# Performance work log

Measured on AMD Instinct MI355X. Metric: run time of the kernel, lower is better.

The kernel has to match this reference:

```python
import jax, jax.numpy as jnp
import numpy as np

B, S, D, H, NL, V, E, DFF = 4, 512, 768, 12, 2, 32000, 8, 3072
CF = 1.25
HD = D // H


def setup_inputs() -> dict:
    key = jax.random.key(0)
    ks = jax.random.split(key, 12)
    r = lambda i, shape: jax.random.normal(ks[i], shape, jnp.float32) * 0.02
    return {
        "src": jax.random.randint(ks[0], (B, S), 0, V),
        "src_pad_mask": jnp.zeros((B, S), bool),
        "emb": r(1, (V, D)),
        "qkv_w": r(2, (NL, 3 * D, D)), "qkv_b": jnp.zeros((NL, 3 * D), jnp.float32),
        "out_w": r(3, (NL, D, D)), "out_b": jnp.zeros((NL, D), jnp.float32),
        "wr": r(4, (NL, D, E)),
        "w1": r(5, (NL, E, D, DFF)), "b1": jnp.zeros((NL, E, DFF), jnp.float32),
        "w2": r(6, (NL, E, DFF, D)), "b2": jnp.zeros((NL, E, D), jnp.float32),
        "ln1_g": jnp.ones((NL, D), jnp.float32), "ln1_b": jnp.zeros((NL, D), jnp.float32),
        "ln2_g": jnp.ones((NL, D), jnp.float32), "ln2_b": jnp.zeros((NL, D), jnp.float32),
        "lnf_g": jnp.ones((D,), jnp.float32), "lnf_b": jnp.zeros((D,), jnp.float32),
    }


def layernorm(x, g, b, eps=1e-5):
    mu = jnp.mean(x, -1, keepdims=True)
    var = jnp.mean((x - mu) ** 2, -1, keepdims=True)
    return (x - mu) * jax.lax.rsqrt(var + eps) * g + b


def pos_encoding():
    pos = jnp.arange(S, dtype=jnp.float32)[:, None]
    i = jnp.arange(0, D, 2, dtype=jnp.float32)
    ang = pos * jnp.exp(-(i / D) * jnp.log(jnp.float32(10000.0)))  # [S, D/2]
    pe = jnp.zeros((S, D), jnp.float32)
    pe = pe.at[:, 0::2].set(jnp.sin(ang)).at[:, 1::2].set(jnp.cos(ang))
    return pe


def mha(x, wqkv, bqkv, wo, bo, pad):
    qkv = x @ wqkv.T + bqkv
    q, k, v = jnp.split(qkv, 3, axis=-1)
    q = q.reshape(B, S, H, HD); k = k.reshape(B, S, H, HD); v = v.reshape(B, S, H, HD)
    sc = jnp.einsum('bqhd,bkhd->bhqk', q, k) * (1.0 / float(HD) ** 0.5)
    sc = jnp.where(pad[:, None, None, :], jnp.float32(-1e9), sc)
    at = jax.nn.softmax(sc, -1)
    o = jnp.einsum('bhqk,bkhd->bqhd', at, v).reshape(B, S, D)
    return o @ wo.T + bo


def switch_ffn(x, token_mask, wr, w1, b1, w2, b2):
    # Switch Transformer top-1 routing with capacity drop.
    T = B * S
    cap = int(CF * T / E)
    xf = x.reshape(T, D)
    vm = token_mask.reshape(T).astype(x.dtype)
    logits = xf @ wr                                   # [T, E]
    probs = jax.nn.softmax(logits, -1)
    idx = jnp.argmax(probs, -1)
    gate = jnp.take_along_axis(probs, idx[:, None], -1)[:, 0]
    oh = jax.nn.one_hot(idx, E, dtype=x.dtype) * vm[:, None]      # [T, E]
    pos = jnp.cumsum(oh, axis=0) * oh                  # 1-indexed position in expert
    keep = ((pos > 0) & (pos <= cap)).astype(x.dtype)
    disp = keep[:, :, None] * jax.nn.one_hot((pos - 1).astype(jnp.int32), cap, dtype=x.dtype)  # [T,E,C]
    comb = disp * gate[:, None, None]
    ein = jnp.einsum('tec,td->ecd', disp, xf)          # [E, C, D]
    hid = jax.nn.relu(jnp.einsum('ecd,edf->ecf', ein, w1) + b1[:, None, :])
    eo = jnp.einsum('ecf,efd->ecd', hid, w2) + b2[:, None, :]
    y = jnp.einsum('tec,ecd->td', comb, eo).reshape(B, S, D)
    denom = jnp.maximum(vm.sum(), 1.0)
    me = (probs * vm[:, None]).sum(0) / denom
    ce = oh.sum(0) / denom
    lb = jnp.float32(E) * jnp.sum(me * ce)
    z = jnp.sum((jax.nn.logsumexp(logits, -1) ** 2) * vm) / denom
    return y, lb, z


def forward(src, src_pad_mask, emb, qkv_w, qkv_b, out_w, out_b, wr, w1, b1, w2, b2,
            ln1_g, ln1_b, ln2_g, ln2_b, lnf_g, lnf_b):
    x = emb[src] * jnp.float32(float(D) ** 0.5) + pos_encoding()[None]
    token_mask = ~src_pad_mask
    lbs, zs = [], []
    for l in range(NL):
        xn = layernorm(x, ln1_g[l], ln1_b[l])
        x = x + mha(xn, qkv_w[l], qkv_b[l], out_w[l], out_b[l], src_pad_mask)
        xn = layernorm(x, ln2_g[l], ln2_b[l])
        y, lb, z = switch_ffn(xn, token_mask, wr[l], w1[l], b1[l], w2[l], b2[l])
        x = x + y
        lbs.append(lb); zs.append(z)
    x = layernorm(x, lnf_g, lnf_b)
    return x, jnp.stack(lbs).mean(), jnp.stack(zs).mean()


def reference(src, src_pad_mask, emb, qkv_w, qkv_b, out_w, out_b, wr, w1, b1, w2, b2,
              ln1_g, ln1_b, ln2_g, ln2_b, lnf_g, lnf_b):
    return forward(src, src_pad_mask, emb, qkv_w, qkv_b, out_w, out_b, wr, w1, b1, w2, b2,
                   ln1_g, ln1_b, ln2_g, ln2_b, lnf_g, lnf_b)
```

## Files before the change

kernel.cpp:

```cpp
#include <hip/hip_runtime.h>

#define BB 4
#define SS 512
#define DD 768
#define HH 12
#define NLAYER 2
#define EE 8
#define DFF 3072
#define TT 2048
#define CAP 320
#define HD 64

typedef unsigned short u16;
typedef long long ll;
typedef _Float16 f16x8 __attribute__((ext_vector_type(8)));
typedef float f32x4 __attribute__((ext_vector_type(4)));

union F16U { _Float16 h; u16 u; };

__device__ __forceinline__ void split2h(float v, u16& h0, u16& h1) {
    F16U c0; c0.h = (_Float16)v;
    float r = (v - (float)c0.h) * 4096.0f;
    F16U c1; c1.h = (_Float16)r;
    h0 = c0.u; h1 = c1.u;
}
__device__ __forceinline__ float rec2h(u16 a, u16 b) {
    F16U c0, c1; c0.u = a; c1.u = b;
    return (float)c0.h + (float)c1.h * (1.0f / 4096.0f);
}

#define MFMA16(a, b, c) __builtin_amdgcn_mfma_f32_16x16x32_f16(a, b, c, 0, 0, 0)

struct GemmP {
    const u16* A = nullptr; ll sAp = 0;
    const void* B = nullptr; ll sBp = 0;
    const float* bias = nullptr; ll biasStride = 0;
    void* C = nullptr; ll sCp = 0;
    int M = 0, N = 0, K = 0, lda = 0, ldb = 0, ldc = 0;
    int modA = 1; ll sA1 = 0, sA2 = 0;
    int modB = 1; ll sB1 = 0, sB2 = 0;
    int modC = 1; ll sC1 = 0, sC2 = 0;
    float alpha = 1.f;
    int flags = 0;
    int KS = 1; ll partStride = 0;
    int Jc = 1;
};

#define BK 64
#define PADK 72

template<bool BTRANS, int NS>
__global__ __launch_bounds__(256) void gemm_kernel(GemmP p) {
    __shared__ u16 Al[NS][128][PADK];
    __shared__ u16 Bl[NS][128][PADK];
    const int tid = threadIdx.x;

    int bx, by, bz;
    {
        int gx = gridDim.x, gy = gridDim.y;
        int NBt = gx * gy * gridDim.z;
        int L = blockIdx.x + gx * (blockIdx.y + gy * blockIdx.z);
        int q = NBt >> 3, r = NBt & 7;
        int xcd = L & 7, wi = L >> 3;
        int c = (xcd < r) ? xcd * (q + 1) + wi : r * (q + 1) + (xcd - r) * q + wi;
        int Jc = p.Jc;
        int gxJ = gx * Jc;
        int sj = c / gxJ;
        int t = c - sj * gxJ;
        bx = t / Jc;
        int j = sj * Jc + (t - (t / Jc) * Jc);
        by = j % gy; bz = j / gy;
    }
    const int n0 = bx * 128, m0 = by * 128;
    const int slice = bz % p.KS;
    const int z = bz / p.KS;
    const int kslice = p.K / p.KS;
    const int k0 = slice * kslice;
    const int nkt = kslice >> 6;

    const u16* Ap = p.A + (ll)(z % p.modA) * p.sA1 + (ll)(z / p.modA) * p.sA2 + k0;
    const ll zB = (ll)(z % p.modB) * p.sB1 + (ll)(z / p.modB) * p.sB2;
    const ll zC = (ll)(z % p.modC) * p.sC1 + (ll)(z / p.modC) * p.sC2;
    const u16* Bpu = BTRANS ? ((const u16*)p.B + zB + k0) : nullptr;
    const float* Bpf = BTRANS ? nullptr : ((const float*)p.B + zB);

    const int lane = tid & 63, wid = tid >> 6;
    const int wm = (wid >> 1) * 64, wn = (wid & 1) * 64;
    const int ar = lane & 15, kg = (lane >> 4) * 8;

    f32x4 acc0[4][4] = {};
    f32x4 acc1[4][4] = {};

    uint4 ra[4 * NS];
    uint4 rb[4 * NS];
    float rbf[32];

    auto loadA = [&](int kt) {
        #pragma unroll
        for (int s = 0; s < NS; ++s)
            #pragma unroll
            for (int h = 0; h < 4; ++h) {
                int c = tid + h * 256, row = c >> 3, q = c & 7;
                int gm = m0 + row;
                uint4 v = {0u, 0u, 0u, 0u};
                if (gm < p.M) v = *(const uint4*)(Ap + (ll)s * p.sAp + (size_t)gm * p.lda + kt * BK + q * 8);
                ra[s * 4 + h] = v;
            }
    };
    auto storeA = [&]() {
        #pragma unroll
        for (int s = 0; s < NS; ++s)
            #pragma unroll
            for (int h = 0; h < 4; ++h) {
                int c = tid + h * 256, row = c >> 3, q = c & 7;
                *(uint4*)&Al[s][row][q * 8] = ra[s * 4 + h];
            }
    };
    auto loadB = [&](int kt) {
        if (BTRANS) {
            #pragma unroll
            for (int s = 0; s < NS; ++s)
                #pragma unroll
                for (int h = 0; h < 4; ++h) {
                    int c = tid + h * 256, row = c >> 3, q = c & 7;
                    int gn = n0 + row;
                    uint4 v = {0u, 0u, 0u, 0u};
                    if (gn < p.N) v = *(const uint4*)(Bpu + (ll)s * p.sBp + (size_t)gn * p.ldb + kt * BK + q * 8);
                    rb[s * 4 + h] = v;
                }
        } else {
            int gn = n0 + (tid & 127);
            int kb = (tid >> 7) * 32;
            #pragma unroll
            for (int i = 0; i < 32; ++i) {
                float v = 0.f;
                if (gn < p.N) v = Bpf[(size_t)(k0 + kt * BK + kb + i) * p.ldb + gn];
                rbf[i] = v;
            }
        }
    };
    auto storeB = [&]() {
        if (BTRANS) {
            #pragma unroll
            for (int s = 0; s < NS; ++s)
                #pragma unroll
                for (int h = 0; h < 4; ++h) {
                    int c = tid + h * 256, row = c >> 3, q = c & 7;
                    *(uint4*)&Bl[s][row][q * 8] = rb[s * 4 + h];
                }
        } else {
            int col = tid & 127;
            int kb = (tid >> 7) * 32;
            #pragma unroll
            for (int i = 0; i < 8; ++i) {
                u16 t0[4], t1[4];
                #pragma unroll
                for (int e = 0; e < 4; ++e) split2h(rbf[i * 4 + e], t0[e], t1[e]);
                *(uint2*)&Bl[0][col][kb + i * 4] = *(uint2*)t0;
                if (NS == 2) *(uint2*)&Bl[1][col][kb + i * 4] = *(uint2*)t1;
            }
        }
    };

    loadA(0); loadB(0);
    for (int kt = 0; kt < nkt; ++kt) {
        storeA(); storeB();
        __syncthreads();
        if (kt + 1 < nkt) { loadA(kt + 1); loadB(kt + 1); }
        #pragma unroll
        for (int kt2 = 0; kt2 < 2; ++kt2) {
            f16x8 b0r[4], b1r[4];
            #pragma unroll
            for (int j = 0; j < 4; ++j) {
                b0r[j] = *(const f16x8*)&Bl[0][wn + j * 16 + ar][kt2 * 32 + kg];
                if (NS == 2) b1r[j] = *(const f16x8*)&Bl[1][wn + j * 16 + ar][kt2 * 32 + kg];
            }
            #pragma unroll
            for (int i = 0; i < 4; ++i) {
                f16x8 a0 = *(const f16x8*)&Al[0][wm + i * 16 + ar][kt2 * 32 + kg];
                f16x8 a1;
                if (NS == 2) a1 = *(const f16x8*)&Al[1][wm + i * 16 + ar][kt2 * 32 + kg];
                #pragma unroll
                for (int j = 0; j < 4; ++j) {
                    acc0[i][j] = MFMA16(a0, b0r[j], acc0[i][j]);
                    if (NS == 2) {
                        acc1[i][j] = MFMA16(a0, b1r[j], acc1[i][j]);
                        acc1[i][j] = MFMA16(a1, b0r[j], acc1[i][j]);
                    }
                }
            }
        }
        __syncthreads();
    }

    const bool doPart = (p.flags & 16);
    float* Cpart = doPart ? ((float*)p.C + (ll)slice * p.partStride + zC) : nullptr;
    const float* biasp = (p.flags & 1) ? (p.bias + (ll)z * p.biasStride) : nullptr;
    u16* C0 = (!doPart && (p.flags & 8)) ? ((u16*)p.C + zC) : nullptr;
    u16* C1 = C0 ? (C0 + p.sCp) : nullptr;
    float* Cf = (!doPart && !(p.flags & 8)) ? ((float*)p.C + zC) : nullptr;
    #pragma unroll
    for (int i = 0; i < 4; ++i) {
        #pragma unroll
        for (int j = 0; j < 4; ++j) {
            int gc = n0 + wn + j * 16 + (lane & 15);
            if (gc >= p.N) continue;
            int gr0 = m0 + wm + i * 16 + (lane >> 4) * 4;
            #pragma unroll
            for (int r = 0; r < 4; ++r) {
                int gr = gr0 + r;
                if (gr >= p.M) continue;
                float v = acc0[i][j][r];
                if (NS == 2) v += acc1[i][j][r] * (1.0f / 4096.0f);
                v *= p.alpha;
                size_t off = (size_t)gr * p.ldc + gc;
                if (doPart) { Cpart[off] = v; continue; }
                if (p.flags & 1) v = __fadd_rn(v, biasp[gc]);
                if (p.flags & 2) v = fmaxf(v, 0.f);
                if (p.flags & 8) { u16 h0, h1; split2h(v, h0, h1); C0[off] = h0; C1[off] = h1; }
                else Cf[off] = v;
            }
        }
    }
}

struct WtP {
    const float* in; u16* out;
    int R, C;
    ll sIn, sOutZ, planeStride;
    int np;
};
__global__ void wtrans_kernel(WtP p) {
    __shared__ float t[32][33];
    int z = blockIdx.z;
    const float* in = p.in + (ll)z * p.sIn;
    u16* out = p.out + (ll)z * p.sOutZ;
    int c0 = blockIdx.x * 32, r0 = blockIdx.y * 32;
    int tx = threadIdx.x, ty = threadIdx.y;
    #pragma unroll
    for (int i = 0; i < 32; i += 8)
        t[ty + i][tx] = in[(size_t)(r0 + ty + i) * p.C + c0 + tx];
    __syncthreads();
    #pragma unroll
    for (int i = 0; i < 32; i += 8) {
        float v = t[tx][ty + i];
        size_t o = (size_t)(c0 + ty + i) * p.R + r0 + tx;
        u16 h0, h1; split2h(v, h0, h1);
        out[o] = h0;
        if (p.np == 2) out[o + p.planeStride] = h1;
    }
}

__global__ __launch_bounds__(256) void flash_kernel(
    const u16* __restrict__ qkvp, ll sQp,
    const u16* __restrict__ vTp, ll sVp,
    const unsigned char* __restrict__ pad,
    u16* __restrict__ attnp, ll sOp) {
    __shared__ u16 KV[2][64][72];
    __shared__ u16 Pl[2][4][16][72];

    int L = blockIdx.x;
    int c = (L & 7) * 48 + (L >> 3);
    int bh = c >> 3, qt = c & 7;
    int b = bh / HH, h = bh % HH;
    int lane = threadIdx.x & 63, wv = threadIdx.x >> 6;
    int qbase = b * SS + qt * 64 + wv * 16;

    int spl = threadIdx.x >> 7;
    int srr = threadIdx.x & 127;
    int srow = srr >> 1, shalf = srr & 1;

    f16x8 qf[2][2];
    {
        const u16* qr = qkvp + (size_t)(qbase + (lane & 15)) * (3 * DD) + h * HD + (lane >> 4) * 8;
        #pragma unroll
        for (int kt2 = 0; kt2 < 2; ++kt2)
            #pragma unroll
            for (int pl = 0; pl < 2; ++pl)
                qf[kt2][pl] = *(const f16x8*)(qr + (ll)pl * sQp + kt2 * 32);
    }

    f32x4 S[32];
    #pragma unroll
    for (int kv = 0; kv < 8; ++kv) {
        const u16* gk = qkvp + (size_t)(b * SS + kv * 64 + srow) * (3 * DD) + DD + h * HD + (ll)spl * sQp;
        #pragma unroll
        for (int qq = 0; qq < 4; ++qq) {
            int off = shalf * 32 + qq * 8;
            *(uint4*)&KV[spl][srow][off] = *(const uint4*)(gk + off);
        }
        __syncthreads();
        #pragma unroll
        for (int nf = 0; nf < 4; ++nf) {
            f32x4 a0 = {}, a1 = {};
            #pragma unroll
            for (int kt2 = 0; kt2 < 2; ++kt2) {
                f16x8 b0 = *(const f16x8*)&KV[0][nf * 16 + (lane & 15)][kt2 * 32 + (lane >> 4) * 8];
                f16x8 b1 = *(const f16x8*)&KV[1][nf * 16 + (lane & 15)][kt2 * 32 + (lane >> 4) * 8];
                a0 = MFMA16(qf[kt2][0], b0, a0);
                a1 = MFMA16(qf[kt2][0], b1, a1);
                a1 = MFMA16(qf[kt2][1], b0, a1);
            }
            int col = kv * 64 + nf * 16 + (lane & 15);
            bool msk = pad[b * SS + col] != 0;
            #pragma unroll
            for (int r = 0; r < 4; ++r) {
                float v = (a0[r] + a1[r] * (1.0f / 4096.0f)) * 0.125f;
                S[kv * 4 + nf][r] = msk ? -1e9f : v;
            }
        }
        __syncthreads();
    }

    float mx[4] = {-1e30f, -1e30f, -1e30f, -1e30f}, sm[4] = {0.f, 0.f, 0.f, 0.f}, inv[4];
    #pragma unroll
    for (int f = 0; f < 32; ++f)
        #pragma unroll
        for (int r = 0; r < 4; ++r) mx[r] = fmaxf(mx[r], S[f][r]);
    #pragma unroll
    for (int r = 0; r < 4; ++r) {
        #pragma unroll
        for (int off = 1; off < 16; off <<= 1) mx[r] = fmaxf(mx[r], __shfl_xor(mx[r], off));
    }
    #pragma unroll
    for (int f = 0; f < 32; ++f)
        #pragma unroll
        for (int r = 0; r < 4; ++r) { float e = expf(S[f][r] - mx[r]); S[f][r] = e; sm[r] += e; }
    #pragma unroll
    for (int r = 0; r < 4; ++r) {
        #pragma unroll
        for (int off = 1; off < 16; off <<= 1) sm[r] += __shfl_xor(sm[r], off);
        inv[r] = 1.f / sm[r];
    }

    f32x4 p0[4] = {}, p1[4] = {};
    #pragma unroll
    for (int kv = 0; kv < 8; ++kv) {
        const u16* gv = vTp + (size_t)bh * HD * SS + (size_t)srow * SS + kv * 64 + (ll)spl * sVp;
        #pragma unroll
        for (int qq = 0; qq < 4; ++qq) {
            int off = shalf * 32 + qq * 8;
            *(uint4*)&KV[spl][srow][off] = *(const uint4*)(gv + off);
        }
        #pragma unroll
        for (int nf = 0; nf < 4; ++nf)
            #pragma unroll
            for (int r = 0; r < 4; ++r) {
                float v = S[kv * 4 + nf][r] * inv[r];
                u16 h0, h1; split2h(v, h0, h1);
                Pl[0][wv][(lane >> 4) * 4 + r][nf * 16 + (lane & 15)] = h0;
                Pl[1][wv][(lane >> 4) * 4 + r][nf * 16 + (lane & 15)] = h1;
            }
        __syncthreads();
        f16x8 pa[2][2];
        #pragma unroll
        for (int kt2 = 0; kt2 < 2; ++kt2)
            #pragma unroll
            for (int pl = 0; pl < 2; ++pl)
                pa[kt2][pl] = *(const f16x8*)&Pl[pl][wv][lane & 15][kt2 * 32 + (lane >> 4) * 8];
        #pragma unroll
        for (int df = 0; df < 4; ++df) {
            #pragma unroll
            for (int kt2 = 0; kt2 < 2; ++kt2) {
                f16x8 v0 = *(const f16x8*)&KV[0][df * 16 + (lane & 15)][kt2 * 32 + (lane >> 4) * 8];
                f16x8 v1 = *(const f16x8*)&KV[1][df * 16 + (lane & 15)][kt2 * 32 + (lane >> 4) * 8];
                p0[df] = MFMA16(pa[kt2][0], v0, p0[df]);
                p1[df] = MFMA16(pa[kt2][0], v1, p1[df]);
                p1[df] = MFMA16(pa[kt2][1], v0, p1[df]);
            }
        }
        __syncthreads();
    }

    #pragma unroll
    for (int df = 0; df < 4; ++df)
        #pragma unroll
        for (int r = 0; r < 4; ++r) {
            float v = p0[df][r] + p1[df][r] * (1.0f / 4096.0f);
            int row = qbase + (lane >> 4) * 4 + r;
            int col = h * HD + df * 16 + (lane & 15);
            u16 h0, h1; split2h(v, h0, h1);
            attnp[(size_t)row * DD + col] = h0;
            attnp[(size_t)row * DD + col + sOp] = h1;
        }
}

struct RedP {
    const float* part = nullptr; ll partStride = 0; int KS = 1;
    float* outf = nullptr;
    u16* o0 = nullptr; ll planeStride = 0;
    const float* bias = nullptr; ll biasStride = 0; ll batchElems = 1; int Nc = 1;
    const float* src = nullptr;
    ll total = 0; int mode = 0;
};
__global__ void reduce_kernel(RedP p) {
    ll e0 = ((ll)blockIdx.x * 256 + threadIdx.x) * 4;
    if (e0 >= p.total) return;
    float4 s = *(const float4*)(p.part + e0);
    for (int k = 1; k < p.KS; ++k) {
        float4 t = *(const float4*)(p.part + (ll)k * p.partStride + e0);
        s.x += t.x; s.y += t.y; s.z += t.z; s.w += t.w;
    }
    if (p.mode & 1) {
        ll b = e0 / p.batchElems;
        int d = (int)(e0 % p.Nc);
        float4 bv = *(const float4*)(p.bias + b * p.biasStride + d);
        s.x = __fadd_rn(s.x, bv.x); s.y = __fadd_rn(s.y, bv.y);
        s.z = __fadd_rn(s.z, bv.z); s.w = __fadd_rn(s.w, bv.w);
    }
    if (p.mode & 4) {
        float4 t = *(const float4*)(p.src + e0);
        s.x = __fadd_rn(s.x, t.x); s.y = __fadd_rn(s.y, t.y);
        s.z = __fadd_rn(s.z, t.z); s.w = __fadd_rn(s.w, t.w);
    }
    if (p.mode & 2) { s.x = fmaxf(s.x, 0.f); s.y = fmaxf(s.y, 0.f); s.z = fmaxf(s.z, 0.f); s.w = fmaxf(s.w, 0.f); }
    if (p.mode & 8) {
        u16 t0[4], t1[4];
        float vv[4] = {s.x, s.y, s.z, s.w};
        #pragma unroll
        for (int e = 0; e < 4; ++e) split2h(vv[e], t0[e], t1[e]);
        *(uint2*)(p.o0 + e0) = *(uint2*)t0;
        *(uint2*)(p.o0 + p.planeStride + e0) = *(uint2*)t1;
    } else {
        *(float4*)(p.outf + e0) = s;
    }
}

__global__ void wsplit_kernel(const float* __restrict__ w, u16* __restrict__ p0,
                              ll planeStride, ll total) {
    ll e0 = ((ll)blockIdx.x * 256 + threadIdx.x) * 4;
    if (e0 >= total) return;
    float4 v = *(const float4*)(w + e0);
    u16 t0[4], t1[4];
    float vv[4] = {v.x, v.y, v.z, v.w};
    #pragma unroll
    for (int e = 0; e < 4; ++e) split2h(vv[e], t0[e], t1[e]);
    *(uint2*)(p0 + e0) = *(uint2*)t0;
    *(uint2*)(p0 + planeStride + e0) = *(uint2*)t1;
}

__global__ void vtrans_kernel(const u16* __restrict__ qkvp, ll sQp,
                              u16* __restrict__ vTp, ll sVp) {
    __shared__ float t[32][33];
    int z = blockIdx.z;
    int b = z / HH, h = z % HH;
    int c0 = blockIdx.x * 32, r0 = blockIdx.y * 32;
    int tx = threadIdx.x, ty = threadIdx.y;
    const u16* in = qkvp + (size_t)(b * SS) * (3 * DD) + 2 * DD + h * HD;
    #pragma unroll
    for (int i = 0; i < 32; i += 8) {
        size_t o = (size_t)(r0 + ty + i) * (3 * DD) + c0 + tx;
        t[ty + i][tx] = rec2h(in[o], in[o + sQp]);
    }
    __syncthreads();
    u16* out = vTp + (size_t)z * HD * SS;
    #pragma unroll
    for (int i = 0; i < 32; i += 8) {
        size_t o = (size_t)(c0 + ty + i) * SS + r0 + tx;
        u16 h0, h1; split2h(t[tx][ty + i], h0, h1);
        out[o] = h0; out[o + sVp] = h1;
    }
}

__global__ void pe_kernel(float* __restrict__ pe) {
    int s = blockIdx.x, tid = threadIdx.x;
    const float lg = 9.210340371976184f;
    #pragma unroll
    for (int j = 0; j < 3; ++j) {
        int d = j * 256 + tid;
        int half = d >> 1;
        float fi = (float)(2 * half) / 768.0f;
        float arg = __fmul_rn(-fi, lg);
        float freq = (float)exp((double)arg);
        float ang = __fmul_rn((float)s, freq);
        double da = (double)ang;
        pe[(size_t)s * DD + d] = (d & 1) ? (float)cos(da) : (float)sin(da);
    }
}

__global__ void embed_kernel(const int* __restrict__ src, const float* __restrict__ emb,
                             const float* __restrict__ pe, float* __restrict__ x) {
    int t = blockIdx.x, tid = threadIdx.x;
    int s = t & (SS - 1);
    int tok = src[t];
    const float sq = 27.712812921102035f;
    #pragma unroll
    for (int j = 0; j < 3; ++j) {
        int d = j * 256 + tid;
        float e = emb[(size_t)tok * DD + d];
        x[(size_t)t * DD + d] = __fadd_rn(__fmul_rn(e, sq), pe[(size_t)s * DD + d]);
    }
}

__global__ void ln_kernel(const float* __restrict__ x, const float* __restrict__ g,
                          const float* __restrict__ b, float* __restrict__ outf,
                          u16* __restrict__ op, ll planeStride) {
    int t = blockIdx.x, tid = threadIdx.x;
    const float* xr = x + (size_t)t * DD;
    float v[3], s = 0.f, sq = 0.f;
    #pragma unroll
    for (int j = 0; j < 3; ++j) { v[j] = xr[tid + j * 256]; s += v[j]; sq += v[j] * v[j]; }
    #pragma unroll
    for (int off = 32; off; off >>= 1) { s += __shfl_xor(s, off); sq += __shfl_xor(sq, off); }
    __shared__ float rs[4], rq[4];
    int wid = tid >> 6;
    if ((tid & 63) == 0) { rs[wid] = s; rq[wid] = sq; }
    __syncthreads();
    s = rs[0] + rs[1] + rs[2] + rs[3];
    sq = rq[0] + rq[1] + rq[2] + rq[3];
    float mu = s / 768.0f;
    float var = sq / 768.0f - mu * mu;
    float rstd = rsqrtf(var + 1e-5f);
    #pragma unroll
    for (int j = 0; j < 3; ++j) {
        int d = tid + j * 256;
        float y = __fadd_rn(__fmul_rn(__fmul_rn(v[j] - mu, rstd), g[d]), b[d]);
        if (outf) outf[(size_t)t * DD + d] = y;
        if (op) {
            size_t o = (size_t)t * DD + d;
            u16 h0, h1; split2h(y, h0, h1);
            op[o] = h0; op[o + planeStride] = h1;
        }
    }
}

__global__ void ln2_router_kernel(const float* __restrict__ x, const float* __restrict__ g,
                                  const float* __restrict__ b, const float* __restrict__ wr,
                                  const unsigned char* __restrict__ pad,
                                  u16* __restrict__ op, ll planeStride,
                                  float* __restrict__ probs, float* __restrict__ lsev,
                                  float* __restrict__ gate, int* __restrict__ idx) {
    int t = blockIdx.x, tid = threadIdx.x;
    const float* xr = x + (size_t)t * DD;
    float v[3], s = 0.f, sq = 0.f;
    #pragma unroll
    for (int j = 0; j < 3; ++j) { v[j] = xr[tid + j * 256]; s += v[j]; sq += v[j] * v[j]; }
    #pragma unroll
    for (int off = 32; off; off >>= 1) { s += __shfl_xor(s, off); sq += __shfl_xor(sq, off); }
    __shared__ float rs[4], rq[4];
    __shared__ float ra[4][8];
    int wid = tid >> 6;
    if ((tid & 63) == 0) { rs[wid] = s; rq[wid] = sq; }
    __syncthreads();
    s = rs[0] + rs[1] + rs[2] + rs[3];
    sq = rq[0] + rq[1] + rq[2] + rq[3];
    float mu = s / 768.0f;
    float var = sq / 768.0f - mu * mu;
    float rstd = rsqrtf(var + 1e-5f);
    float a[8] = {0.f, 0.f, 0.f, 0.f, 0.f, 0.f, 0.f, 0.f};
    #pragma unroll
    for (int j = 0; j < 3; ++j) {
        int d = tid + j * 256;
        float y = __fadd_rn(__fmul_rn(__fmul_rn(v[j] - mu, rstd), g[d]), b[d]);
        size_t o = (size_t)t * DD + d;
        u16 h0, h1; split2h(y, h0, h1);
        op[o] = h0; op[o + planeStride] = h1;
        const float* w = wr + (size_t)d * EE;
        #pragma unroll
        for (int e = 0; e < 8; ++e) a[e] += y * w[e];
    }
    #pragma unroll
    for (int off = 32; off; off >>= 1)
        #pragma unroll
        for (int e = 0; e < 8; ++e) a[e] += __shfl_xor(a[e], off);
    if ((tid & 63) == 0)
        #pragma unroll
        for (int e = 0; e < 8; ++e) ra[wid][e] = a[e];
    __syncthreads();
    if (tid == 0) {
        #pragma unroll
        for (int e = 0; e < 8; ++e) a[e] = ra[0][e] + ra[1][e] + ra[2][e] + ra[3][e];
        int vm = (pad[t] == 0);
        float mx = a[0]; int bi = 0;
        #pragma unroll
        for (int e = 1; e < 8; ++e) if (a[e] > mx) { mx = a[e]; bi = e; }
        float ex[8], sum = 0.f;
        #pragma unroll
        for (int e = 0; e < 8; ++e) { ex[e] = expf(a[e] - mx); sum += ex[e]; }
        float inv = 1.f / sum;
        #pragma unroll
        for (int e = 0; e < 8; ++e) probs[(size_t)t * EE + e] = vm ? ex[e] * inv : 0.f;
        lsev[t] = vm ? (mx + logf(sum)) : 0.f;
        gate[t] = ex[bi] * inv;
        idx[t] = vm ? bi : -1;
    }
}

__global__ void route_scan_kernel(const int* __restrict__ idx, const float* __restrict__ probs,
                                  const float* __restrict__ lsev, int* __restrict__ slot,
                                  int* __restrict__ tos, float* __restrict__ acc) {
    int lane = threadIdx.x;
    int base = lane * 32;
    int ev[32];
    int c[8] = {0, 0, 0, 0, 0, 0, 0, 0};
    #pragma unroll
    for (int i = 0; i < 32; ++i) {
        int e = idx[base + i];
        ev[i] = e;
        #pragma unroll
        for (int q = 0; q < 8; ++q) c[q] += (e == q);
    }
    int excl[8], tot[8];
    #pragma unroll
    for (int e = 0; e < 8; ++e) {
        int v = c[e];
        #pragma unroll
        for (int off = 1; off < 64; off <<= 1) {
            int n = __shfl_up(v, off);
            if (lane >= off) v += n;
        }
        excl[e] = v - c[e];
        tot[e] = __shfl(v, 63);
    }
    int r[8];
    #pragma unroll
    for (int e = 0; e < 8; ++e) r[e] = excl[e];
    #pragma unroll
    for (int i = 0; i < 32; ++i) {
        int t = base + i, e = ev[i], s = -1;
        if (e >= 0) {
            int pos = 0;
            #pragma unroll
            for (int q = 0; q < 8; ++q) if (e == q) { r[q]++; pos = r[q]; }
            if (pos <= CAP) { s = e * CAP + pos - 1; tos[s] = t; }
        }
        slot[t] = s;
    }
    float pa[8] = {0.f, 0.f, 0.f, 0.f, 0.f, 0.f, 0.f, 0.f};
    float l2 = 0.f, vld = 0.f;
    #pragma unroll
    for (int i = 0; i < 32; ++i) {
        int t = base + i;
        float lv = lsev[t];
        l2 += lv * lv;
        if (ev[i] >= 0) vld += 1.f;
        #pragma unroll
        for (int e = 0; e < 8; ++e) pa[e] += probs[(size_t)t * EE + e];
    }
    #pragma unroll
    for (int off = 32; off; off >>= 1) {
        #pragma unroll
        for (int e = 0; e < 8; ++e) pa[e] += __shfl_xor(pa[e], off);
        l2 += __shfl_xor(l2, off);
        vld += __shfl_xor(vld, off);
    }
    if (lane == 0) {
        float denom = fmaxf(vld, 1.f);
        float lb = 0.f;
        #pragma unroll
        for (int e = 0; e < 8; ++e) lb += (pa[e] / denom) * ((float)tot[e] / denom);
        lb *= 8.f;
        acc[0] += lb;
        acc[1] += l2 / denom;
    }
}

__global__ void gather_kernel(const int* __restrict__ tos, const u16* __restrict__ xnp,
                              ll sXp, u16* __restrict__ einp, ll sEp) {
    int s = blockIdx.x;
    int tid = threadIdx.x;
    if (tid >= 192) return;
    int pl = tid / 96, q = tid % 96;
    int t = tos[s];
    uint4 v = {0u, 0u, 0u, 0u};
    if (t >= 0) v = *(const uint4*)(xnp + (ll)pl * sXp + (size_t)t * DD + q * 8);
    *(uint4*)(einp + (ll)pl * sEp + (size_t)s * DD + q * 8) = v;
}

__global__ void combine2_kernel(const int* __restrict__ slot, const float* __restrict__ gate,
                                const float* __restrict__ part, ll partStride, int KS,
                                const float* __restrict__ b2, float* __restrict__ x) {
    int t = blockIdx.x, tid = threadIdx.x;
    int s = slot[t];
    if (s < 0) return;
    float gv = gate[t];
    int e = s / CAP;
    #pragma unroll
    for (int j = 0; j < 3; ++j) {
        int d = j * 256 + tid;
        size_t o = (size_t)s * DD + d;
        float v = part[o];
        for (int k = 1; k < KS; ++k) v += part[(ll)k * partStride + o];
        v = __fadd_rn(v, b2[(size_t)e * DD + d]);
        size_t ox = (size_t)t * DD + d;
        x[ox] = __fadd_rn(x[ox], __fmul_rn(gv, v));
    }
}

__global__ void finalize_kernel(const float* __restrict__ acc, float* __restrict__ out) {
    out[(size_t)TT * DD] = acc[0] * (1.f / NLAYER);
    out[(size_t)TT * DD + 1] = acc[1] * (1.f / NLAYER);
}

static inline void run_gemm(bool btrans, int ns, const GemmP& p, dim3 grid, hipStream_t s) {
    if (btrans) {
        if (ns == 2) gemm_kernel<true, 2><<<grid, 256, 0, s>>>(p);
        else gemm_kernel<true, 1><<<grid, 256, 0, s>>>(p);
    } else {
        if (ns == 2) gemm_kernel<false, 2><<<grid, 256, 0, s>>>(p);
        else gemm_kernel<false, 1><<<grid, 256, 0, s>>>(p);
    }
}
static inline void run_reduce(const RedP& r, hipStream_t s) {
    reduce_kernel<<<(int)((r.total / 4 + 255) / 256), 256, 0, s>>>(r);
}

extern "C" void kernel_launch(void* const* d_in, const int* in_sizes, int n_in,
                              void* d_out, int out_size, void* d_ws, size_t ws_size,
                              hipStream_t stream) {
    const int* src = (const int*)d_in[0];
    const unsigned char* pad = (const unsigned char*)d_in[1];
    const float* emb = (const float*)d_in[2];
    const float* qkv_w = (const float*)d_in[3];
    const float* qkv_b = (const float*)d_in[4];
    const float* out_w = (const float*)d_in[5];
    const float* out_b = (const float*)d_in[6];
    const float* wr = (const float*)d_in[7];
    const float* w1 = (const float*)d_in[8];
    const float* b1 = (const float*)d_in[9];
    const float* w2 = (const float*)d_in[10];
    const float* b2 = (const float*)d_in[11];
    const float* ln1_g = (const float*)d_in[12];
    const float* ln1_b = (const float*)d_in[13];
    const float* ln2_g = (const float*)d_in[14];
    const float* ln2_b = (const float*)d_in[15];
    const float* lnf_g = (const float*)d_in[16];
    const float* lnf_b = (const float*)d_in[17];

    char* w = (char*)d_ws;
    size_t off = 0;
    auto alloc = [&](size_t bytes) -> void* {
        void* p = w + off;
        off += (bytes + 255) & ~(size_t)255;
        return p;
    };
    float* x      = (float*)alloc((size_t)TT * DD * 4);
    float* peT    = (float*)alloc((size_t)SS * DD * 4);
    u16*   xnp    = (u16*)  alloc((size_t)2 * TT * DD * 2);
    u16*   qkvp   = (u16*)  alloc((size_t)2 * TT * 3 * DD * 2);
    u16*   vTp    = (u16*)  alloc((size_t)2 * BB * HH * HD * SS * 2);
    u16*   attnp  = (u16*)  alloc((size_t)2 * TT * DD * 2);
    u16*   einp   = (u16*)  alloc((size_t)2 * EE * CAP * DD * 2);
    u16*   hidp   = (u16*)  alloc((size_t)2 * EE * CAP * DFF * 2);
    char*  regB   = (char*) alloc((size_t)2 * TT * 3 * DD * 4);
    u16*   qkvwp  = (u16*)  alloc((size_t)2 * NLAYER * 3 * DD * DD * 2);
    u16*   owp    = (u16*)  alloc((size_t)2 * NLAYER * DD * DD * 2);
    float* probs  = (float*)alloc((size_t)TT * EE * 4);
    float* lsev   = (float*)alloc((size_t)TT * 4);
    float* gate   = (float*)alloc((size_t)TT * 4);
    int*   idx    = (int*)  alloc((size_t)TT * 4);
    int*   slot   = (int*)  alloc((size_t)TT * 4);
    int*   tos    = (int*)  alloc((size_t)EE * CAP * 4);
    float* accb   = (float*)alloc(256);
    if (off > ws_size) return;
    u16* w1Tp = (u16*)alloc((size_t)2 * EE * DFF * DD * 2);
    u16* w2Tp = (u16*)alloc((size_t)2 * EE * DD * DFF * 2);
    const bool use_tr = (off <= ws_size);

    float* qkvpart = (float*)regB;
    float* oppart  = (float*)regB;
    float* ffnpart = (float*)regB;

    hipMemsetAsync(accb, 0, 8, stream);
    pe_kernel<<<SS, 256, 0, stream>>>(peT);
    embed_kernel<<<TT, 256, 0, stream>>>(src, emb, peT, x);

    {
        ll tq = (ll)NLAYER * 3 * DD * DD;
        wsplit_kernel<<<(int)((tq / 4 + 255) / 256), 256, 0, stream>>>(qkv_w, qkvwp, tq, tq);
        ll to = (ll)NLAYER * DD * DD;
        wsplit_kernel<<<(int)((to / 4 + 255) / 256), 256, 0, stream>>>(out_w, owp, to, to);
    }

    for (int l = 0; l < NLAYER; ++l) {
        const int nsF = (l < NLAYER - 1) ? 2 : 1;
        ln_kernel<<<TT, 256, 0, stream>>>(x, ln1_g + l * DD, ln1_b + l * DD, nullptr, xnp, (ll)TT * DD);

        {
            GemmP p;
            p.A = xnp; p.sAp = (ll)TT * DD; p.lda = DD;
            p.B = qkvwp + (size_t)l * 3 * DD * DD; p.sBp = (ll)NLAYER * 3 * DD * DD; p.ldb = DD;
            p.C = qkvpart; p.ldc = 3 * DD;
            p.M = TT; p.N = 3 * DD; p.K = DD;
            p.flags = 16; p.KS = 2; p.partStride = (ll)TT * 3 * DD;
            p.Jc = 4;
            run_gemm(true, 2, p, dim3(18, 16, 2), stream);
        }
        {
            RedP r;
            r.part = qkvpart; r.partStride = (ll)TT * 3 * DD; r.KS = 2;
            r.o0 = qkvp; r.planeStride = (ll)TT * 3 * DD;
            r.bias = qkv_b + (size_t)l * 3 * DD; r.biasStride = 0; r.batchElems = (ll)TT * 3 * DD; r.Nc = 3 * DD;
            r.total = (ll)TT * 3 * DD; r.mode = 1 | 8;
            run_reduce(r, stream);
        }
        vtrans_kernel<<<dim3(HD / 32, SS / 32, BB * HH), dim3(32, 8), 0, stream>>>(
            qkvp, (ll)TT * 3 * DD, vTp, (ll)BB * HH * HD * SS);
        flash_kernel<<<BB * HH * 8, 256, 0, stream>>>(
            qkvp, (ll)TT * 3 * DD, vTp, (ll)BB * HH * HD * SS, pad, attnp, (ll)TT * DD);
        {
            GemmP p;
            p.A = attnp; p.sAp = (ll)TT * DD; p.lda = DD;
            p.B = owp + (size_t)l * DD * DD; p.sBp = (ll)NLAYER * DD * DD; p.ldb = DD;
            p.C = oppart; p.ldc = DD;
            p.M = TT; p.N = DD; p.K = DD;
            p.flags = 16; p.KS = 4; p.partStride = (ll)TT * DD;
            p.Jc = 8;
            run_gemm(true, 2, p, dim3(6, 16, 4), stream);
        }
        {
            RedP r;
            r.part = oppart; r.partStride = (ll)TT * DD; r.KS = 4;
            r.outf = x;
            r.bias = out_b + (size_t)l * DD; r.biasStride = 0; r.batchElems = (ll)TT * DD; r.Nc = DD;
            r.src = x;
            r.total = (ll)TT * DD; r.mode = 1 | 4;
            run_reduce(r, stream);
        }
        ln2_router_kernel<<<TT, 256, 0, stream>>>(x, ln2_g + l * DD, ln2_b + l * DD,
                                                  wr + (size_t)l * DD * EE, pad,
                                                  xnp, (ll)TT * DD, probs, lsev, gate, idx);
        hipMemsetAsync(tos, 0xFF, (size_t)EE * CAP * 4, stream);
        route_scan_kernel<<<1, 64, 0, stream>>>(idx, probs, lsev, slot, tos, accb);
        gather_kernel<<<EE * CAP, 256, 0, stream>>>(tos, xnp, (ll)TT * DD, einp, (ll)EE * CAP * DD);
        if (use_tr) {
            WtP t1; t1.in = w1 + (size_t)l * EE * DD * DFF; t1.out = w1Tp;
            t1.R = DD; t1.C = DFF; t1.sIn = (ll)DD * DFF; t1.sOutZ = (ll)DFF * DD;
            t1.planeStride = (ll)EE * DFF * DD; t1.np = nsF;
            wtrans_kernel<<<dim3(DFF / 32, DD / 32, EE), dim3(32, 8), 0, stream>>>(t1);
            WtP t2; t2.in = w2 + (size_t)l * EE * DFF * DD; t2.out = w2Tp;
            t2.R = DFF; t2.C = DD; t2.sIn = (ll)DFF * DD; t2.sOutZ = (ll)DD * DFF;
            t2.planeStride = (ll)EE * DD * DFF; t2.np = nsF;
            wtrans_kernel<<<dim3(DD / 32, DFF / 32, EE), dim3(32, 8), 0, stream>>>(t2);
        }
        {
            GemmP p;
            p.A = einp; p.sAp = (ll)EE * CAP * DD; p.lda = DD;
            p.modA = EE; p.sA1 = (ll)CAP * DD;
            p.bias = b1 + (size_t)l * EE * DFF; p.biasStride = DFF;
            p.C = hidp; p.sCp = (ll)EE * CAP * DFF; p.ldc = DFF;
            p.modC = EE; p.sC1 = (ll)CAP * DFF;
            p.M = CAP; p.N = DFF; p.K = DD;
            p.flags = 1 | 2 | 8;
            p.Jc = 3;
            if (use_tr) {
                p.B = w1Tp; p.sBp = (ll)EE * DFF * DD; p.ldb = DD;
                p.modB = EE; p.sB1 = (ll)DFF * DD;
                run_gemm(true, nsF, p, dim3(24, 3, EE), stream);
            } else {
                p.B = w1 + (size_t)l * EE * DD * DFF; p.ldb = DFF;
                p.modB = EE; p.sB1 = (ll)DD * DFF;
                run_gemm(false, nsF, p, dim3(24, 3, EE), stream);
            }
        }
        {
            GemmP p;
            p.A = hidp; p.sAp = (ll)EE * CAP * DFF; p.lda = DFF;
            p.modA = EE; p.sA1 = (ll)CAP * DFF;
            p.C = ffnpart; p.ldc = DD; p.modC = EE; p.sC1 = (ll)CAP * DD;
            p.M = CAP; p.N = DD; p.K = DFF;
            p.flags = 16; p.KS = 4; p.partStride = (ll)EE * CAP * DD;
            p.Jc = 12;
            if (use_tr) {
                p.B = w2Tp; p.sBp = (ll)EE * DD * DFF; p.ldb = DFF;
                p.modB = EE; p.sB1 = (ll)DD * DFF;
                run_gemm(true, nsF, p, dim3(6, 3, EE * 4), stream);
            } else {
                p.B = w2 + (size_t)l * EE * DFF * DD; p.ldb = DD;
                p.modB = EE; p.sB1 = (ll)DFF * DD;
                run_gemm(false, nsF, p, dim3(6, 3, EE * 4), stream);
            }
        }
        combine2_kernel<<<TT, 256, 0, stream>>>(slot, gate, ffnpart, (ll)EE * CAP * DD, 4,
                                                b2 + (size_t)l * EE * DD, x);
    }
    ln_kernel<<<TT, 256, 0, stream>>>(x, lnf_g, lnf_b, (float*)d_out, nullptr, 0);
    finalize_kernel<<<1, 1, 0, stream>>>(accb, (float*)d_out);
}
```

Measured before the change: 841.2 us.

## Load GEMM A operand fragments directly from global memory, bypassing LDS

The A tile is no longer staged through shared memory. Each wave now loads its MFMA A fragments straight from global memory inside the inner k loop. This removes LDS stores and reads for A and halves LDS usage, which may raise occupancy. In exchange the two wn-waves issue duplicate global loads for the same rows, the loads are small strided 16-byte reads with no prefetch, and global latency now sits directly in front of the MFMAs.

```diff
diff --git a/kernel.cpp b/kernel.cpp
--- a/kernel.cpp
+++ b/kernel.cpp
@@ -51,7 +51,6 @@
 
 template<bool BTRANS, int NS>
 __global__ __launch_bounds__(256) void gemm_kernel(GemmP p) {
-    __shared__ u16 Al[NS][128][PADK];
     __shared__ u16 Bl[NS][128][PADK];
     const int tid = threadIdx.x;
 
@@ -91,31 +90,12 @@
     f32x4 acc0[4][4] = {};
     f32x4 acc1[4][4] = {};
 
-    uint4 ra[4 * NS];
     uint4 rb[4 * NS];
     float rbf[32];
 
-    auto loadA = [&](int kt) {
-        #pragma unroll
-        for (int s = 0; s < NS; ++s)
-            #pragma unroll
-            for (int h = 0; h < 4; ++h) {
-                int c = tid + h * 256, row = c >> 3, q = c & 7;
-                int gm = m0 + row;
-                uint4 v = {0u, 0u, 0u, 0u};
-                if (gm < p.M) v = *(const uint4*)(Ap + (ll)s * p.sAp + (size_t)gm * p.lda + kt * BK + q * 8);
-                ra[s * 4 + h] = v;
-            }
-    };
-    auto storeA = [&]() {
-        #pragma unroll
-        for (int s = 0; s < NS; ++s)
-            #pragma unroll
-            for (int h = 0; h < 4; ++h) {
-                int c = tid + h * 256, row = c >> 3, q = c & 7;
-                *(uint4*)&Al[s][row][q * 8] = ra[s * 4 + h];
-            }
-    };
+    const int arow0 = m0 + wm + ar;
+    const u16* Abase = Ap + (size_t)arow0 * p.lda + kg;
+
     auto loadB = [&](int kt) {
         if (BTRANS) {
             #pragma unroll
@@ -162,13 +142,22 @@
         }
     };
 
-    loadA(0); loadB(0);
+    loadB(0);
     for (int kt = 0; kt < nkt; ++kt) {
-        storeA(); storeB();
+        storeB();
         __syncthreads();
-        if (kt + 1 < nkt) { loadA(kt + 1); loadB(kt + 1); }
+        if (kt + 1 < nkt) loadB(kt + 1);
         #pragma unroll
         for (int kt2 = 0; kt2 < 2; ++kt2) {
+            f16x8 af0[4], af1[4];
+            #pragma unroll
+            for (int i = 0; i < 4; ++i) {
+                int row = arow0 + i * 16;
+                const u16* a = Abase + (size_t)i * 16 * p.lda + kt * BK + kt2 * 32;
+                f16x8 z8 = {};
+                af0[i] = (row < p.M) ? *(const f16x8*)a : z8;
+                if (NS == 2) af1[i] = (row < p.M) ? *(const f16x8*)(a + p.sAp) : z8;
+            }
             f16x8 b0r[4], b1r[4];
             #pragma unroll
             for (int j = 0; j < 4; ++j) {
@@ -177,15 +166,12 @@
             }
             #pragma unroll
             for (int i = 0; i < 4; ++i) {
-                f16x8 a0 = *(const f16x8*)&Al[0][wm + i * 16 + ar][kt2 * 32 + kg];
-                f16x8 a1;
-                if (NS == 2) a1 = *(const f16x8*)&Al[1][wm + i * 16 + ar][kt2 * 32 + kg];
                 #pragma unroll
                 for (int j = 0; j < 4; ++j) {
-                    acc0[i][j] = MFMA16(a0, b0r[j], acc0[i][j]);
+                    acc0[i][j] = MFMA16(af0[i], b0r[j], acc0[i][j]);
                     if (NS == 2) {
-                        acc1[i][j] = MFMA16(a0, b1r[j], acc1[i][j]);
-                        acc1[i][j] = MFMA16(a1, b0r[j], acc1[i][j]);
+                        acc1[i][j] = MFMA16(af0[i], b1r[j], acc1[i][j]);
+                        acc1[i][j] = MFMA16(af1[i], b0r[j], acc1[i][j]);
                     }
                 }
             }
```

Result: slower. 991.6 us (+17.9%).
